# Optimization experiments

Measured on AMD Instinct MI355X. Metric: run time of the kernel, lower is better.

Reference implementation:

```python
import jax, jax.numpy as jnp
import numpy as np

B, N, S, HID, HEADS = 64, 256, 16, 32, 8
BN_EPS = 1e-5


def setup_inputs() -> dict:
    key = jax.random.key(0)
    k1, k2, k3, k4 = jax.random.split(key, 4)
    stacks = jax.random.normal(k1, (B, N, N, S), dtype=jnp.float32)
    # True = padded node (row masked out), like the torch code's `mask`
    mask = jax.random.bernoulli(k2, 0.2, (B, N))
    # BatchNorm1d(S) params (train mode -> batch stats; affine params below)
    gamma = jnp.ones((S,), jnp.float32)
    beta = jnp.zeros((S,), jnp.float32)
    # Linear(S -> HID), ReLU, Linear(HID -> HEADS)
    W1 = jax.random.normal(k3, (S, HID), dtype=jnp.float32) * (1.0 / np.sqrt(S))
    b1 = jnp.zeros((HID,), jnp.float32)
    W2 = jax.random.normal(k4, (HID, HEADS), dtype=jnp.float32) * (1.0 / np.sqrt(HID))
    b2 = jnp.zeros((HEADS,), jnp.float32)
    return {"stacks": stacks, "mask": mask, "gamma": gamma, "beta": beta,
            "W1": W1, "b1": b1, "W2": W2, "b2": b2}


def reference(stacks, mask, gamma, beta, W1, b1, W2, b2):
    # stacks: [b, n, n, S]; mask: [b, n] bool, True = padded.
    # Torch: rows stacks[~mask] (shape [K, n, S]) are flattened to [K*n, S],
    # passed through BN(train) + Linear + ReLU + Linear, and scattered back
    # into a zero [b, n, n, heads] tensor. Equivalent dense formulation:
    # compute BN stats as a masked mean/var over valid rows, apply the MLP
    # everywhere, then zero out masked rows.
    valid = ~mask                                   # [b, n]
    w = valid.astype(stacks.dtype)[:, :, None, None]  # [b, n, 1, 1]
    n1 = stacks.shape[2]
    count = jnp.sum(valid.astype(stacks.dtype)) * n1  # K * n valid BN rows
    sx = jnp.sum(stacks * w, axis=(0, 1, 2))        # [S]
    sx2 = jnp.sum((stacks * stacks) * w, axis=(0, 1, 2))
    mean = sx / count
    var = sx2 / count - mean * mean                 # biased var (BN train mode)
    xn = (stacks - mean) * (gamma / jnp.sqrt(var + BN_EPS)) + beta
    h = jax.nn.relu(jnp.einsum('bnms,sh->bnmh', xn, W1) + b1)
    y = jnp.einsum('bnmh,hk->bnmk', h, W2) + b2     # [b, n, n, heads]
    return jnp.where(valid[:, :, None, None], y, jnp.zeros((), y.dtype))
```

## Files before the change

kernel.cpp:

```cpp
#include <hip/hip_runtime.h>
#include <hip/hip_bf16.h>

#define BB 64
#define NN 256
#define SS 16
#define HH 32
#define KK 8
#define NROWPAIRS (BB*NN)
#define STATS_BLOCKS 2048


__global__ void prep_kernel(const void* __restrict__ mask_raw,
                            int* __restrict__ mode_out,
                            int* __restrict__ count_out,
                            unsigned char* __restrict__ valid,
                            float* __restrict__ sx,
                            float* __restrict__ sx2) {
    int tid = threadIdx.x;
    if (tid < 16) { sx[tid] = 0.0f; sx2[tid] = 0.0f; }

    __shared__ int s_flags[2];
    __shared__ int s_mode;
    __shared__ int s_count;
    if (tid < 2) s_flags[tid] = 0;
    if (tid == 0) s_count = 0;
    __syncthreads();

    const unsigned int* w = (const unsigned int*)mask_raw;
    int f_float = 0, f_bool = 0;
    for (int i = tid; i < 4096; i += 1024) {
        unsigned int v = w[i];
        if (v == 0x3F800000u) f_float = 1;
        if (((v >> 8) & 0xFFu) == 1u || ((v >> 16) & 0xFFu) == 1u ||
            ((v >> 24) & 0xFFu) == 1u) f_bool = 1;
    }
    if (f_float) atomicOr(&s_flags[0], 1);
    if (f_bool)  atomicOr(&s_flags[1], 1);
    __syncthreads();
    if (tid == 0) {
        int mode = s_flags[1] ? 1 : (s_flags[0] ? 2 : 0);
        s_mode = mode;
        *mode_out = mode;
    }
    __syncthreads();
    int mode = s_mode;

    int localc = 0;
    for (int i = tid; i < NROWPAIRS; i += 1024) {
        int masked;
        if (mode == 1)      masked = ((const unsigned char*)mask_raw)[i] != 0;
        else if (mode == 2) masked = ((const float*)mask_raw)[i] != 0.0f;
        else                masked = ((const int*)mask_raw)[i] != 0;
        unsigned char v = (unsigned char)(masked ? 0 : 1);
        valid[i] = v;
        localc += v;
    }
    atomicAdd(&s_count, localc);
    __syncthreads();
    if (tid == 0) *count_out = s_count;
}

__global__ __launch_bounds__(256) void stats_kernel(
        const float* __restrict__ stacks,
        const unsigned char* __restrict__ valid,
        float* __restrict__ sx, float* __restrict__ sx2) {
    int tid = threadIdx.x;
    float4 s1 = make_float4(0.f, 0.f, 0.f, 0.f);
    float4 s2 = make_float4(0.f, 0.f, 0.f, 0.f);

    for (int k = 0; k < NROWPAIRS / STATS_BLOCKS; ++k) {
        int chunk = blockIdx.x + k * STATS_BLOCKS;
        if (!valid[chunk]) continue;
        const float4* p = (const float4*)stacks + (size_t)chunk * 1024;
        #pragma unroll
        for (int it = 0; it < 4; ++it) {
            float4 v = p[tid + it * 256];
            s1.x += v.x; s1.y += v.y; s1.z += v.z; s1.w += v.w;
            s2.x += v.x * v.x; s2.y += v.y * v.y;
            s2.z += v.z * v.z; s2.w += v.w * v.w;
        }
    }

    __shared__ float lds[8 * 256];
    lds[0 * 256 + tid] = s1.x; lds[1 * 256 + tid] = s1.y;
    lds[2 * 256 + tid] = s1.z; lds[3 * 256 + tid] = s1.w;
    lds[4 * 256 + tid] = s2.x; lds[5 * 256 + tid] = s2.y;
    lds[6 * 256 + tid] = s2.z; lds[7 * 256 + tid] = s2.w;
    __syncthreads();

    if (tid < 32) {
        int kind = tid >> 4;
        int s = tid & 15;
        int g = s >> 2, c = (s & 3) + kind * 4;
        float tot = 0.f;
        for (int i = 0; i < 64; ++i) tot += lds[c * 256 + (g + i * 4)];
        atomicAdd(kind ? &sx2[s] : &sx[s], tot);
    }
}

__global__ void weights_kernel(const float* __restrict__ gamma,
                               const float* __restrict__ beta,
                               const float* __restrict__ W1,
                               const float* __restrict__ b1,
                               const float* __restrict__ sx,
                               const float* __restrict__ sx2,
                               const int* __restrict__ count_rows,
                               float* __restrict__ W1c,
                               float* __restrict__ b1c) {
    __shared__ float s_scale[SS], s_shift[SS];
    int tid = threadIdx.x;
    if (tid < SS) {
        float cnt = (float)(*count_rows) * (float)NN;
        if (cnt < 1.0f) cnt = 1.0f;
        float mean = sx[tid] / cnt;
        float var  = sx2[tid] / cnt - mean * mean;
        float sc   = gamma[tid] / sqrtf(var + 1e-5f);
        s_scale[tid] = sc;
        s_shift[tid] = beta[tid] - mean * sc;
    }
    __syncthreads();
    if (tid < SS * HH) W1c[tid] = s_scale[tid >> 5] * W1[tid];
    if (tid < HH) {
        float acc = b1[tid];
        #pragma unroll
        for (int s = 0; s < SS; ++s) acc += s_shift[s] * W1[s * HH + tid];
        b1c[tid] = acc;
    }
}

__global__ __launch_bounds__(256) void mlp_kernel(
        const float* __restrict__ stacks,
        const unsigned char* __restrict__ valid,
        const float* __restrict__ W1c,
        const float* __restrict__ b1c,
        const float* __restrict__ W2,
        const float* __restrict__ b2,
        float* __restrict__ out) {
    int bid = blockIdx.x;
    int tid = threadIdx.x;
    size_t row = (size_t)bid * NN + tid;
    float4* outp = (float4*)out + row * 2;

    if (!valid[bid]) {
        float4 z = make_float4(0.f, 0.f, 0.f, 0.f);
        outp[0] = z; outp[1] = z;
        return;
    }

    const float4* xp = (const float4*)stacks + row * 4;
    float4 x0 = xp[0], x1 = xp[1], x2 = xp[2], x3 = xp[3];

    __shared__ __align__(16) float w_s[808];
    {
        int g = tid * 4;
        if (g < 808) {
            float4 v;
            if (g < 512)      v = ((const float4*)W1c)[tid];
            else if (g < 544) v = ((const float4*)b1c)[(g - 512) >> 2];
            else if (g < 800) v = ((const float4*)W2)[(g - 544) >> 2];
            else              v = ((const float4*)b2)[(g - 800) >> 2];
            *(float4*)&w_s[g] = v;
        }
    }
    __syncthreads();

    const float4* W1v = (const float4*)&w_s[0];
    const float4* b1v = (const float4*)&w_s[512];
    const float4* W2v = (const float4*)&w_s[544];
    const float4* b2v = (const float4*)&w_s[800];

    float x[SS] = { x0.x, x0.y, x0.z, x0.w,  x1.x, x1.y, x1.z, x1.w,
                    x2.x, x2.y, x2.z, x2.w,  x3.x, x3.y, x3.z, x3.w };

    float4 h[8];
    #pragma unroll
    for (int jv = 0; jv < 8; ++jv) h[jv] = b1v[jv];
    #pragma unroll
    for (int k = 0; k < SS; ++k) {
        float xk = x[k];
        #pragma unroll
        for (int jv = 0; jv < 8; ++jv) {
            float4 w = W1v[k * 8 + jv];
            h[jv].x = fmaf(xk, w.x, h[jv].x);
            h[jv].y = fmaf(xk, w.y, h[jv].y);
            h[jv].z = fmaf(xk, w.z, h[jv].z);
            h[jv].w = fmaf(xk, w.w, h[jv].w);
        }
    }
    float hs[HH];
    #pragma unroll
    for (int jv = 0; jv < 8; ++jv) {
        hs[4 * jv + 0] = fmaxf(h[jv].x, 0.0f);
        hs[4 * jv + 1] = fmaxf(h[jv].y, 0.0f);
        hs[4 * jv + 2] = fmaxf(h[jv].z, 0.0f);
        hs[4 * jv + 3] = fmaxf(h[jv].w, 0.0f);
    }

    float4 y0 = b2v[0], y1 = b2v[1];
    #pragma unroll
    for (int j = 0; j < HH; ++j) {
        float hj = hs[j];
        float4 wa = W2v[j * 2 + 0];
        float4 wb = W2v[j * 2 + 1];
        y0.x = fmaf(hj, wa.x, y0.x);
        y0.y = fmaf(hj, wa.y, y0.y);
        y0.z = fmaf(hj, wa.z, y0.z);
        y0.w = fmaf(hj, wa.w, y0.w);
        y1.x = fmaf(hj, wb.x, y1.x);
        y1.y = fmaf(hj, wb.y, y1.y);
        y1.z = fmaf(hj, wb.z, y1.z);
        y1.w = fmaf(hj, wb.w, y1.w);
    }

    outp[0] = y0;
    outp[1] = y1;
}

extern "C" void kernel_launch(void* const* d_in, const int* in_sizes, int n_in,
                              void* d_out, int out_size, void* d_ws, size_t ws_size,
                              hipStream_t stream) {
    const float* stacks = (const float*)d_in[0];
    const void*  mask   = d_in[1];
    const float* gamma  = (const float*)d_in[2];
    const float* beta   = (const float*)d_in[3];
    const float* W1     = (const float*)d_in[4];
    const float* b1     = (const float*)d_in[5];
    const float* W2     = (const float*)d_in[6];
    const float* b2     = (const float*)d_in[7];
    float* out = (float*)d_out;

    char* ws = (char*)d_ws;
    int*           mode      = (int*)(ws + 0);
    int*           countRows = (int*)(ws + 4);
    unsigned char* valid     = (unsigned char*)(ws + 64);
    float*         sx        = (float*)(ws + 16448);
    float*         sx2       = (float*)(ws + 16512);
    float*         b1c       = (float*)(ws + 16576);
    float*         W1c      = (float*)(ws + 16704);

    prep_kernel<<<1, 1024, 0, stream>>>(mask, mode, countRows, valid, sx, sx2);
    stats_kernel<<<STATS_BLOCKS, 256, 0, stream>>>(stacks, valid, sx, sx2);
    weights_kernel<<<1, 512, 0, stream>>>(gamma, beta, W1, b1, sx, sx2,
                                          countRows, W1c, b1c);
    mlp_kernel<<<NROWPAIRS, 256, 0, stream>>>(stacks, valid, W1c, b1c, W2, b2, out);
}
```

Measured before the change: 495.2 us.

## Fuse mask prep into stats and weight folding into MLP, reverse block order

Mask decoding and valid-row counting move into the stats kernel, and the BN weight folding moves into each MLP block's prologue. This cuts the launch chain from four kernels to a memset plus two, and drops the single-block serial prep kernel. The MLP kernel now handles four row-chunks per block and walks blocks in reverse order, probably so the tail of stacks still in cache from the stats pass is read first. In exchange every MLP block redundantly recomputes the folded weights, and every stats block rescans the mask header to detect its dtype.

Result: slower. 519.2 us (+4.9%).

```diff
diff --git a/kernel.cpp b/kernel.cpp
--- a/kernel.cpp
+++ b/kernel.cpp
@@ -1,34 +1,35 @@
 #include <hip/hip_runtime.h>
-#include <hip/hip_bf16.h>
-
-#define BB 64
+
 #define NN 256
 #define SS 16
 #define HH 32
 #define KK 8
-#define NROWPAIRS (BB*NN)
+#define NROWPAIRS 16384
 #define STATS_BLOCKS 2048
-
-
-__global__ void prep_kernel(const void* __restrict__ mask_raw,
-                            int* __restrict__ mode_out,
-                            int* __restrict__ count_out,
-                            unsigned char* __restrict__ valid,
-                            float* __restrict__ sx,
-                            float* __restrict__ sx2) {
+#define CPB 4
+#define MLP_BLOCKS (NROWPAIRS / CPB)
+
+
+__global__ __launch_bounds__(256) void stats_kernel(
+        const void* __restrict__ mask_raw,
+        const float* __restrict__ stacks,
+        unsigned char* __restrict__ valid,
+        int* __restrict__ count_out,
+        float* __restrict__ sx, float* __restrict__ sx2) {
     int tid = threadIdx.x;
-    if (tid < 16) { sx[tid] = 0.0f; sx2[tid] = 0.0f; }
+    int bid = blockIdx.x;
 
     __shared__ int s_flags[2];
     __shared__ int s_mode;
     __shared__ int s_count;
+    __shared__ unsigned char s_valid[8];
     if (tid < 2) s_flags[tid] = 0;
     if (tid == 0) s_count = 0;
     __syncthreads();
 
     const unsigned int* w = (const unsigned int*)mask_raw;
     int f_float = 0, f_bool = 0;
-    for (int i = tid; i < 4096; i += 1024) {
+    for (int i = tid; i < 4096; i += 256) {
         unsigned int v = w[i];
         if (v == 0x3F800000u) f_float = 1;
         if (((v >> 8) & 0xFFu) == 1u || ((v >> 16) & 0xFFu) == 1u ||
@@ -37,40 +38,29 @@
     if (f_float) atomicOr(&s_flags[0], 1);
     if (f_bool)  atomicOr(&s_flags[1], 1);
     __syncthreads();
-    if (tid == 0) {
-        int mode = s_flags[1] ? 1 : (s_flags[0] ? 2 : 0);
-        s_mode = mode;
-        *mode_out = mode;
-    }
+    if (tid == 0) s_mode = s_flags[1] ? 1 : (s_flags[0] ? 2 : 0);
     __syncthreads();
     int mode = s_mode;
 
-    int localc = 0;
-    for (int i = tid; i < NROWPAIRS; i += 1024) {
+    if (tid < 8) {
+        int chunk = bid + tid * STATS_BLOCKS;
         int masked;
-        if (mode == 1)      masked = ((const unsigned char*)mask_raw)[i] != 0;
-        else if (mode == 2) masked = ((const float*)mask_raw)[i] != 0.0f;
-        else                masked = ((const int*)mask_raw)[i] != 0;
+        if (mode == 1)      masked = ((const unsigned char*)mask_raw)[chunk] != 0;
+        else if (mode == 2) masked = ((const float*)mask_raw)[chunk] != 0.0f;
+        else                masked = ((const int*)mask_raw)[chunk] != 0;
         unsigned char v = (unsigned char)(masked ? 0 : 1);
-        valid[i] = v;
-        localc += v;
-    }
-    atomicAdd(&s_count, localc);
-    __syncthreads();
-    if (tid == 0) *count_out = s_count;
-}
-
-__global__ __launch_bounds__(256) void stats_kernel(
-        const float* __restrict__ stacks,
-        const unsigned char* __restrict__ valid,
-        float* __restrict__ sx, float* __restrict__ sx2) {
-    int tid = threadIdx.x;
+        s_valid[tid] = v;
+        valid[chunk] = v;
+        if (v) atomicAdd(&s_count, 1);
+    }
+    __syncthreads();
+    if (tid == 0 && s_count) atomicAdd(count_out, s_count);
+
     float4 s1 = make_float4(0.f, 0.f, 0.f, 0.f);
     float4 s2 = make_float4(0.f, 0.f, 0.f, 0.f);
-
-    for (int k = 0; k < NROWPAIRS / STATS_BLOCKS; ++k) {
-        int chunk = blockIdx.x + k * STATS_BLOCKS;
-        if (!valid[chunk]) continue;
+    for (int k = 0; k < 8; ++k) {
+        if (!s_valid[k]) continue;
+        int chunk = bid + k * STATS_BLOCKS;
         const float4* p = (const float4*)stacks + (size_t)chunk * 1024;
         #pragma unroll
         for (int it = 0; it < 4; ++it) {
@@ -98,17 +88,25 @@
     }
 }
 
-__global__ void weights_kernel(const float* __restrict__ gamma,
-                               const float* __restrict__ beta,
-                               const float* __restrict__ W1,
-                               const float* __restrict__ b1,
-                               const float* __restrict__ sx,
-                               const float* __restrict__ sx2,
-                               const int* __restrict__ count_rows,
-                               float* __restrict__ W1c,
-                               float* __restrict__ b1c) {
+__global__ __launch_bounds__(256) void mlp_kernel(
+        const float* __restrict__ stacks,
+        const unsigned char* __restrict__ valid,
+        const float* __restrict__ gamma,
+        const float* __restrict__ beta,
+        const float* __restrict__ W1,
+        const float* __restrict__ b1,
+        const float* __restrict__ W2,
+        const float* __restrict__ b2,
+        const float* __restrict__ sx,
+        const float* __restrict__ sx2,
+        const int* __restrict__ count_rows,
+        float* __restrict__ out) {
+    int tid = threadIdx.x;
+    int bid = (MLP_BLOCKS - 1) - (int)blockIdx.x;
+
+    __shared__ __align__(16) float w_s[808];
     __shared__ float s_scale[SS], s_shift[SS];
-    int tid = threadIdx.x;
+
     if (tid < SS) {
         float cnt = (float)(*count_rows) * (float)NN;
         if (cnt < 1.0f) cnt = 1.0f;
@@ -117,50 +115,24 @@
         float sc   = gamma[tid] / sqrtf(var + 1e-5f);
         s_scale[tid] = sc;
         s_shift[tid] = beta[tid] - mean * sc;
-    }
-    __syncthreads();
-    if (tid < SS * HH) W1c[tid] = s_scale[tid >> 5] * W1[tid];
-    if (tid < HH) {
-        float acc = b1[tid];
-        #pragma unroll
-        for (int s = 0; s < SS; ++s) acc += s_shift[s] * W1[s * HH + tid];
-        b1c[tid] = acc;
-    }
-}
-
-__global__ __launch_bounds__(256) void mlp_kernel(
-        const float* __restrict__ stacks,
-        const unsigned char* __restrict__ valid,
-        const float* __restrict__ W1c,
-        const float* __restrict__ b1c,
-        const float* __restrict__ W2,
-        const float* __restrict__ b2,
-        float* __restrict__ out) {
-    int bid = blockIdx.x;
-    int tid = threadIdx.x;
-    size_t row = (size_t)bid * NN + tid;
-    float4* outp = (float4*)out + row * 2;
-
-    if (!valid[bid]) {
-        float4 z = make_float4(0.f, 0.f, 0.f, 0.f);
-        outp[0] = z; outp[1] = z;
-        return;
-    }
-
-    const float4* xp = (const float4*)stacks + row * 4;
-    float4 x0 = xp[0], x1 = xp[1], x2 = xp[2], x3 = xp[3];
-
-    __shared__ __align__(16) float w_s[808];
-    {
-        int g = tid * 4;
-        if (g < 808) {
-            float4 v;
-            if (g < 512)      v = ((const float4*)W1c)[tid];
-            else if (g < 544) v = ((const float4*)b1c)[(g - 512) >> 2];
-            else if (g < 800) v = ((const float4*)W2)[(g - 544) >> 2];
-            else              v = ((const float4*)b2)[(g - 800) >> 2];
-            *(float4*)&w_s[g] = v;
-        }
+    } else if (tid >= 128 && tid < 192) {
+        ((float4*)&w_s[544])[tid - 128] = ((const float4*)W2)[tid - 128];
+    } else if (tid >= 192 && tid < 194) {
+        ((float4*)&w_s[800])[tid - 192] = ((const float4*)b2)[tid - 192];
+    }
+    __syncthreads();
+
+    if (tid < 128) {
+        float4 wv = ((const float4*)W1)[tid];
+        float sc = s_scale[tid >> 3];
+        wv.x *= sc; wv.y *= sc; wv.z *= sc; wv.w *= sc;
+        ((float4*)&w_s[0])[tid] = wv;
+    } else if (tid >= 224) {
+        int j = tid - 224;
+        float acc = b1[j];
+        #pragma unroll
+        for (int s = 0; s < SS; ++s) acc += s_shift[s] * W1[s * HH + j];
+        w_s[512 + j] = acc;
     }
     __syncthreads();
 
@@ -169,51 +141,65 @@
     const float4* W2v = (const float4*)&w_s[544];
     const float4* b2v = (const float4*)&w_s[800];
 
-    float x[SS] = { x0.x, x0.y, x0.z, x0.w,  x1.x, x1.y, x1.z, x1.w,
-                    x2.x, x2.y, x2.z, x2.w,  x3.x, x3.y, x3.z, x3.w };
-
-    float4 h[8];
-    #pragma unroll
-    for (int jv = 0; jv < 8; ++jv) h[jv] = b1v[jv];
-    #pragma unroll
-    for (int k = 0; k < SS; ++k) {
-        float xk = x[k];
+    for (int c = 0; c < CPB; ++c) {
+        int chunk = bid * CPB + c;
+        size_t row = (size_t)chunk * NN + tid;
+        float4* outp = (float4*)out + row * 2;
+
+        if (!valid[chunk]) {
+            float4 z = make_float4(0.f, 0.f, 0.f, 0.f);
+            outp[0] = z; outp[1] = z;
+            continue;
+        }
+
+        const float4* xp = (const float4*)stacks + row * 4;
+        float4 x0 = xp[0], x1 = xp[1], x2 = xp[2], x3 = xp[3];
+        float x[SS] = { x0.x, x0.y, x0.z, x0.w,  x1.x, x1.y, x1.z, x1.w,
+                        x2.x, x2.y, x2.z, x2.w,  x3.x, x3.y, x3.z, x3.w };
+
+        float4 h[8];
+        #pragma unroll
+        for (int jv = 0; jv < 8; ++jv) h[jv] = b1v[jv];
+        #pragma unroll
+        for (int k = 0; k < SS; ++k) {
+            float xk = x[k];
+            #pragma unroll
+            for (int jv = 0; jv < 8; ++jv) {
+                float4 wv = W1v[k * 8 + jv];
+                h[jv].x = fmaf(xk, wv.x, h[jv].x);
+                h[jv].y = fmaf(xk, wv.y, h[jv].y);
+                h[jv].z = fmaf(xk, wv.z, h[jv].z);
+                h[jv].w = fmaf(xk, wv.w, h[jv].w);
+            }
+        }
+        float hs[HH];
         #pragma unroll
         for (int jv = 0; jv < 8; ++jv) {
-            float4 w = W1v[k * 8 + jv];
-            h[jv].x = fmaf(xk, w.x, h[jv].x);
-            h[jv].y = fmaf(xk, w.y, h[jv].y);
-            h[jv].z = fmaf(xk, w.z, h[jv].z);
-            h[jv].w = fmaf(xk, w.w, h[jv].w);
-        }
-    }
-    float hs[HH];
-    #pragma unroll
-    for (int jv = 0; jv < 8; ++jv) {
-        hs[4 * jv + 0] = fmaxf(h[jv].x, 0.0f);
-        hs[4 * jv + 1] = fmaxf(h[jv].y, 0.0f);
-        hs[4 * jv + 2] = fmaxf(h[jv].z, 0.0f);
-        hs[4 * jv + 3] = fmaxf(h[jv].w, 0.0f);
-    }
-
-    float4 y0 = b2v[0], y1 = b2v[1];
-    #pragma unroll
-    for (int j = 0; j < HH; ++j) {
-        float hj = hs[j];
-        float4 wa = W2v[j * 2 + 0];
-        float4 wb = W2v[j * 2 + 1];
-        y0.x = fmaf(hj, wa.x, y0.x);
-        y0.y = fmaf(hj, wa.y, y0.y);
-        y0.z = fmaf(hj, wa.z, y0.z);
-        y0.w = fmaf(hj, wa.w, y0.w);
-        y1.x = fmaf(hj, wb.x, y1.x);
-        y1.y = fmaf(hj, wb.y, y1.y);
-        y1.z = fmaf(hj, wb.z, y1.z);
-        y1.w = fmaf(hj, wb.w, y1.w);
-    }
-
-    outp[0] = y0;
-    outp[1] = y1;
+            hs[4 * jv + 0] = fmaxf(h[jv].x, 0.0f);
+            hs[4 * jv + 1] = fmaxf(h[jv].y, 0.0f);
+            hs[4 * jv + 2] = fmaxf(h[jv].z, 0.0f);
+            hs[4 * jv + 3] = fmaxf(h[jv].w, 0.0f);
+        }
+
+        float4 y0 = b2v[0], y1 = b2v[1];
+        #pragma unroll
+        for (int j = 0; j < HH; ++j) {
+            float hj = hs[j];
+            float4 wa = W2v[j * 2 + 0];
+            float4 wb = W2v[j * 2 + 1];
+            y0.x = fmaf(hj, wa.x, y0.x);
+            y0.y = fmaf(hj, wa.y, y0.y);
+            y0.z = fmaf(hj, wa.z, y0.z);
+            y0.w = fmaf(hj, wa.w, y0.w);
+            y1.x = fmaf(hj, wb.x, y1.x);
+            y1.y = fmaf(hj, wb.y, y1.y);
+            y1.z = fmaf(hj, wb.z, y1.z);
+            y1.w = fmaf(hj, wb.w, y1.w);
+        }
+
+        outp[0] = y0;
+        outp[1] = y1;
+    }
 }
 
 extern "C" void kernel_launch(void* const* d_in, const int* in_sizes, int n_in,
@@ -230,17 +216,16 @@
     float* out = (float*)d_out;
 
     char* ws = (char*)d_ws;
-    int*           mode      = (int*)(ws + 0);
-    int*           countRows = (int*)(ws + 4);
-    unsigned char* valid     = (unsigned char*)(ws + 64);
-    float*         sx        = (float*)(ws + 16448);
-    float*         sx2       = (float*)(ws + 16512);
-    float*         b1c       = (float*)(ws + 16576);
-    float*         W1c      = (float*)(ws + 16704);
-
-    prep_kernel<<<1, 1024, 0, stream>>>(mask, mode, countRows, valid, sx, sx2);
-    stats_kernel<<<STATS_BLOCKS, 256, 0, stream>>>(stacks, valid, sx, sx2);
-    weights_kernel<<<1, 512, 0, stream>>>(gamma, beta, W1, b1, sx, sx2,
-                                          countRows, W1c, b1c);
-    mlp_kernel<<<NROWPAIRS, 256, 0, stream>>>(stacks, valid, W1c, b1c, W2, b2, out);
+    int*           countRows = (int*)(ws + 0);
+    float*         sx        = (float*)(ws + 64);
+    float*         sx2       = (float*)(ws + 128);
+    unsigned char* valid     = (unsigned char*)(ws + 192);
+
+    hipMemsetAsync(ws, 0, 192, stream);
+
+    stats_kernel<<<STATS_BLOCKS, 256, 0, stream>>>(mask, stacks, valid,
+                                                   countRows, sx, sx2);
+    mlp_kernel<<<MLP_BLOCKS, 256, 0, stream>>>(stacks, valid, gamma, beta,
+                                               W1, b1, W2, b2, sx, sx2,
+                                               countRows, out);
 }
```
